# Optimization experiments

Hardware: AMD Instinct MI355X
Metric: run time of the kernel (lower is better)

The kernel has to match this reference:

```python
import jax, jax.numpy as jnp
import numpy as np

D_MODEL = 1024
N_HEADS = 16
D_HEAD = D_MODEL // N_HEADS


def setup_inputs() -> dict:
    key = jax.random.key(0)
    ks = jax.random.split(key, 9)
    B, S = 2, 2048
    s = 0.02
    return {
        "x": jax.random.normal(ks[0], (B, S, D_MODEL), dtype=jnp.float32),
        "Wq": jax.random.normal(ks[1], (D_MODEL, D_MODEL), dtype=jnp.float32) * s,
        "bq": jnp.zeros((D_MODEL,), dtype=jnp.float32),
        "Wk": jax.random.normal(ks[2], (D_MODEL, D_MODEL), dtype=jnp.float32) * s,
        "bk": jnp.zeros((D_MODEL,), dtype=jnp.float32),
        "Wv": jax.random.normal(ks[3], (D_MODEL, D_MODEL), dtype=jnp.float32) * s,
        "bv": jnp.zeros((D_MODEL,), dtype=jnp.float32),
        "Wo": jax.random.normal(ks[4], (D_MODEL, D_MODEL), dtype=jnp.float32) * s,
        "bo": jnp.zeros((D_MODEL,), dtype=jnp.float32),
    }


def reference(x, Wq, bq, Wk, bk, Wv, bv, Wo, bo):
    B, S, _ = x.shape
    # projections -> [B, H, S, Dh]
    def split_heads(t):
        return t.reshape(B, S, N_HEADS, D_HEAD).transpose(0, 2, 1, 3)
    Q = split_heads(x @ Wq + bq)
    K = split_heads(x @ Wk + bk)
    V = split_heads(x @ Wv + bv)
    scores = jnp.einsum('bhqd,bhkd->bhqk', Q, K)  # [B,H,S,S]
    mask = jnp.tril(jnp.ones((S, S), dtype=bool))
    # NB: original masks BEFORE scaling (mask fill -1e9 then /sqrt(d_head))
    scores = jnp.where(mask[None, None], scores, jnp.float32(-1e9))
    scores = scores / jnp.sqrt(jnp.float32(D_HEAD))
    attn = jax.nn.softmax(scores, axis=-1)
    ctx = jnp.einsum('bhqk,bhkd->bhqd', attn, V)
    ctx = ctx.transpose(0, 2, 1, 3).reshape(B, S, D_MODEL)
    return ctx @ Wo + bo
```

## Files before the change

kernel.cpp:

```cpp
#include <hip/hip_runtime.h>

typedef __bf16 bf16;
typedef __bf16 bf16x8 __attribute__((ext_vector_type(8)));
typedef __bf16 bf16x4 __attribute__((ext_vector_type(4)));
typedef float  f32x4  __attribute__((ext_vector_type(4)));

#define D_MODEL 1024
#define S_LEN   2048
#define NHEAD   16
#define DHEAD   64
#define BATCH   2
#define MROWS   (BATCH * S_LEN)

#define QSCALE 0.18033688011112042f

__device__ __forceinline__ void gld_lds16(const void* g, void* lds_base) {
    __builtin_amdgcn_global_load_lds(
        (const __attribute__((address_space(1))) void*)g,
        (__attribute__((address_space(3))) void*)lds_base, 16, 0, 0);
}

__global__ void prep_kernel(const float* __restrict__ x,
                            const float* __restrict__ W0, const float* __restrict__ W1,
                            const float* __restrict__ W2, const float* __restrict__ W3,
                            bf16* __restrict__ xb, bf16* __restrict__ Wt) {
    int tx = threadIdx.x, ty = threadIdx.y;
    if (blockIdx.z == 4) {
        int tid = ty * 32 + tx;
        size_t base = ((size_t)blockIdx.y * 32 + blockIdx.x) * 4096 + (size_t)tid * 16;
        f32x4 v0 = *(const f32x4*)(x + base);
        f32x4 v1 = *(const f32x4*)(x + base + 4);
        f32x4 v2 = *(const f32x4*)(x + base + 8);
        f32x4 v3 = *(const f32x4*)(x + base + 12);
        bf16x8 o0, o1;
#pragma unroll
        for (int r = 0; r < 4; r++) {
            o0[r] = (bf16)v0[r]; o0[r + 4] = (bf16)v1[r];
            o1[r] = (bf16)v2[r]; o1[r + 4] = (bf16)v3[r];
        }
        *(bf16x8*)(xb + base)     = o0;
        *(bf16x8*)(xb + base + 8) = o1;
        return;
    }
    __shared__ float tile[32][33];
    const float* W = (blockIdx.z == 0) ? W0 : (blockIdx.z == 1) ? W1
                   : (blockIdx.z == 2) ? W2 : W3;
    int n0 = blockIdx.x * 32, k0 = blockIdx.y * 32;
#pragma unroll
    for (int j = 0; j < 4; j++)
        tile[ty + 8 * j][tx] = W[(size_t)(k0 + ty + 8 * j) * D_MODEL + n0 + tx];
    __syncthreads();
    bf16* out = Wt + (size_t)blockIdx.z * D_MODEL * D_MODEL;
    int nn = ty + 8 * (tx >> 3);
    int k4 = (tx & 7) * 4;
    bf16x4 pk;
#pragma unroll
    for (int r = 0; r < 4; r++) pk[r] = (bf16)tile[k4 + r][nn];
    *(bf16x4*)(out + (size_t)(n0 + nn) * D_MODEL + k0 + k4) = pk;
}

template <int MODE>
__global__ __launch_bounds__(256, 3) void gemm_kernel(
    const bf16* __restrict__ A, const bf16* __restrict__ Bt,
    const float* __restrict__ b0, const float* __restrict__ b1, const float* __restrict__ b2,
    bf16* __restrict__ Qo, bf16* __restrict__ Ko, bf16* __restrict__ Vto,
    float* __restrict__ Co) {
    __shared__ bf16 sA[3][128 * 32];
    __shared__ bf16 sB[3][128 * 32];
    const int t = threadIdx.x;
    const int wave = t >> 6, lane = t & 63;
    const int wm = wave >> 1, wn = wave & 1;
    const int quad = lane >> 4, m16 = lane & 15;
    const int row0 = blockIdx.y * 128, col0 = blockIdx.x * 128;
    const int K = D_MODEL;
    const int NT = K / 32;

    f32x4 acc[4][4];
#pragma unroll
    for (int i = 0; i < 4; i++)
#pragma unroll
        for (int j = 0; j < 4; j++) acc[i][j] = (f32x4){0.f, 0.f, 0.f, 0.f};

    auto stage = [&](int j, int buf) {
#pragma unroll
        for (int i = 0; i < 2; i++) {
            int cb = i * 256 + wave * 64;
            int c  = cb + lane;
            int r  = c >> 2, kg = c & 3;
            gld_lds16(A  + (size_t)(row0 + r) * K + j * 32 + kg * 8,
                      (char*)&sA[buf][0] + cb * 16);
            gld_lds16(Bt + (size_t)(col0 + r) * K + j * 32 + kg * 8,
                      (char*)&sB[buf][0] + cb * 16);
        }
    };

    stage(0, 0);
    stage(1, 1);

    for (int j = 0; j < NT; ++j) {
        if (j + 1 < NT) asm volatile("s_waitcnt vmcnt(4)\n\ts_barrier" ::: "memory");
        else            asm volatile("s_waitcnt vmcnt(0)\n\ts_barrier" ::: "memory");
        if (j + 2 < NT) stage(j + 2, (j + 2) % 3);
        const int cur = j % 3;

        bf16x8 af[4], bfr[4];
#pragma unroll
        for (int mi = 0; mi < 4; mi++)
            af[mi] = *(const bf16x8*)&sA[cur][(wm * 64 + mi * 16 + m16) * 32 + quad * 8];
#pragma unroll
        for (int ni = 0; ni < 4; ni++)
            bfr[ni] = *(const bf16x8*)&sB[cur][(wn * 64 + ni * 16 + m16) * 32 + quad * 8];
#pragma unroll
        for (int mi = 0; mi < 4; mi++)
#pragma unroll
            for (int ni = 0; ni < 4; ni++)
                acc[mi][ni] = __builtin_amdgcn_mfma_f32_16x16x32_bf16(
                    af[mi], bfr[ni], acc[mi][ni], 0, 0, 0);
    }

    if (MODE == 1) {
#pragma unroll
        for (int mi = 0; mi < 4; mi++) {
            int r0 = row0 + wm * 64 + mi * 16 + quad * 4;
#pragma unroll
            for (int ni = 0; ni < 4; ni++) {
                int col = col0 + wn * 64 + ni * 16 + m16;
                float bias = b0[col];
#pragma unroll
                for (int r = 0; r < 4; r++)
                    Co[(size_t)(r0 + r) * D_MODEL + col] = acc[mi][ni][r] + bias;
            }
        }
    } else {
        int sel = col0 >> 10;
        const float* bias_arr = (sel == 0) ? b0 : (sel == 1) ? b1 : b2;
#pragma unroll
        for (int mi = 0; mi < 4; mi++) {
            int s0g = row0 + wm * 64 + mi * 16 + quad * 4;
            int b = s0g >> 11, ss0 = s0g & 2047;
#pragma unroll
            for (int ni = 0; ni < 4; ni++) {
                int col = col0 + wn * 64 + ni * 16 + m16;
                int cn = col & 1023;
                int h = cn >> 6, d = cn & 63;
                float bias = bias_arr[cn];
                if (sel < 2) {
                    bf16* dst = (sel == 0) ? Qo : Ko;
                    float scl = (sel == 0) ? QSCALE : 1.0f;
                    size_t base = (((size_t)b * NHEAD + h) * S_LEN);
#pragma unroll
                    for (int r = 0; r < 4; r++)
                        dst[(base + ss0 + r) * DHEAD + d] = (bf16)((acc[mi][ni][r] + bias) * scl);
                } else {
                    bf16x4 pk;
#pragma unroll
                    for (int r = 0; r < 4; r++) pk[r] = (bf16)(acc[mi][ni][r] + bias);
                    *(bf16x4*)(Vto + (((size_t)b * NHEAD + h) * DHEAD + d) * S_LEN + ss0) = pk;
                }
            }
        }
    }
}

__global__ __launch_bounds__(256, 2) void attn_kernel(
    const bf16* __restrict__ Q, const bf16* __restrict__ K,
    const bf16* __restrict__ Vt, bf16* __restrict__ ctx) {
    __shared__ bf16 Kt_s[3][64 * 64];
    __shared__ bf16 Vt_s[3][64 * 64];
    __shared__ bf16 P_s[4][2][16 * 72];

    const int t = threadIdx.x, wave = t >> 6, lane = t & 63;
    const int quad = lane >> 4, m16 = lane & 15;
    const int bh = blockIdx.y, p = blockIdx.x;
    const int tT[2] = {p, 31 - p};
    const int nt = 32 - p;
    const size_t base = (size_t)bh * S_LEN * DHEAD;

    bf16x8 aq[2][2];
#pragma unroll
    for (int it = 0; it < 2; it++)
#pragma unroll
        for (int kst = 0; kst < 2; kst++)
            aq[it][kst] = *(const bf16x8*)(Q + base
                + (size_t)(tT[it] * 64 + wave * 16 + m16) * DHEAD + kst * 32 + quad * 8);

    f32x4 o[2][4];
#pragma unroll
    for (int it = 0; it < 2; it++)
#pragma unroll
        for (int di = 0; di < 4; di++) o[it][di] = (f32x4){0.f, 0.f, 0.f, 0.f};
    float l_acc[2] = {0.f, 0.f};

    auto stage = [&](int j, int buf) {
#pragma unroll
        for (int i = 0; i < 2; i++) {
            int cb = i * 256 + wave * 64;
            int c  = cb + lane;
            int pos = c >> 3, g = c & 7;
            int gk = g ^ (pos & 7);
            gld_lds16(K  + base + (size_t)(j * 64 + pos) * DHEAD + gk * 8,
                      (char*)&Kt_s[buf][0] + cb * 16);
            gld_lds16(Vt + base + (size_t)pos * S_LEN + j * 64 + gk * 8,
                      (char*)&Vt_s[buf][0] + cb * 16);
        }
    };

    stage(0, 0);
    if (nt > 1) stage(1, 1);

    for (int j = 0; j < nt; ++j) {
        if (j + 1 < nt) asm volatile("s_waitcnt vmcnt(4)\n\ts_barrier" ::: "memory");
        else            asm volatile("s_waitcnt vmcnt(0)\n\ts_barrier" ::: "memory");
        if (j + 2 < nt) stage(j + 2, (j + 2) % 3);

        const int cur = j % 3;
        const bool aAct = (j <= tT[0]);
        const int kt0 = j * 64;

        auto computeTile = [&](bool both) {
            int itlo = both ? 0 : 1;
            f32x4 sc[2][4];
#pragma unroll
            for (int it = 0; it < 2; it++)
#pragma unroll
                for (int ni = 0; ni < 4; ni++) sc[it][ni] = (f32x4){0.f, 0.f, 0.f, 0.f};
#pragma unroll
            for (int ni = 0; ni < 4; ni++) {
                int pos = ni * 16 + m16;
#pragma unroll
                for (int kst = 0; kst < 2; kst++) {
                    int gg = (kst * 4 + quad) ^ (pos & 7);
                    bf16x8 kf = *(const bf16x8*)&Kt_s[cur][pos * 64 + gg * 8];
                    sc[1][ni] = __builtin_amdgcn_mfma_f32_16x16x32_bf16(
                        kf, aq[1][kst], sc[1][ni], 0, 0, 0);
                    if (both)
                        sc[0][ni] = __builtin_amdgcn_mfma_f32_16x16x32_bf16(
                            kf, aq[0][kst], sc[0][ni], 0, 0, 0);
                }
            }
#pragma unroll
            for (int it = 0; it < 2; it++) {
                if (it < itlo) continue;
                if (j == tT[it]) {
                    int qg = tT[it] * 64 + wave * 16 + m16;
#pragma unroll
                    for (int ni = 0; ni < 4; ni++)
#pragma unroll
                        for (int r = 0; r < 4; r++) {
                            int kp = kt0 + ni * 16 + quad * 4 + r;
                            if (kp > qg) sc[it][ni][r] = -1e9f;
                        }
                }
            }
#pragma unroll
            for (int it = 0; it < 2; it++) {
                if (it < itlo) continue;
                bf16* Pw = &P_s[wave][it][0];
                float ls = 0.f;
#pragma unroll
                for (int ni = 0; ni < 4; ni++) {
                    bf16x4 pk;
#pragma unroll
                    for (int r = 0; r < 4; r++) {
                        float pe = __builtin_amdgcn_exp2f(sc[it][ni][r]);
                        ls += pe;
                        pk[r] = (bf16)pe;
                    }
                    *(bf16x4*)&Pw[m16 * 72 + ni * 16 + quad * 4] = pk;
                }
                l_acc[it] += ls;
            }
#pragma unroll
            for (int kst = 0; kst < 2; kst++) {
                bf16x8 ap[2];
#pragma unroll
                for (int it = 0; it < 2; it++)
                    if (it >= itlo)
                        ap[it] = *(const bf16x8*)&P_s[wave][it][m16 * 72 + kst * 32 + quad * 8];
#pragma unroll
                for (int di = 0; di < 4; di++) {
                    int d = di * 16 + m16;
                    int gg = (kst * 4 + quad) ^ (d & 7);
                    bf16x8 vf = *(const bf16x8*)&Vt_s[cur][d * 64 + gg * 8];
                    o[1][di] = __builtin_amdgcn_mfma_f32_16x16x32_bf16(
                        vf, ap[1], o[1][di], 0, 0, 0);
                    if (both)
                        o[0][di] = __builtin_amdgcn_mfma_f32_16x16x32_bf16(
                            vf, ap[0], o[0][di], 0, 0, 0);
                }
            }
        };
        if (aAct) computeTile(true);
        else      computeTile(false);
    }

    int b = bh >> 4, h = bh & 15;
#pragma unroll
    for (int it = 0; it < 2; it++) {
        float l = l_acc[it];
        l += __shfl_xor(l, 16);
        l += __shfl_xor(l, 32);
        float rl = 1.0f / l;
        int s = tT[it] * 64 + wave * 16 + m16;
#pragma unroll
        for (int di = 0; di < 4; di++) {
            bf16x4 pk;
#pragma unroll
            for (int r = 0; r < 4; r++) pk[r] = (bf16)(o[it][di][r] * rl);
            *(bf16x4*)(ctx + ((size_t)b * S_LEN + s) * D_MODEL
                       + h * DHEAD + di * 16 + quad * 4) = pk;
        }
    }
}

extern "C" void kernel_launch(void* const* d_in, const int* in_sizes, int n_in,
                              void* d_out, int out_size, void* d_ws, size_t ws_size,
                              hipStream_t stream) {
    const float* x  = (const float*)d_in[0];
    const float* Wq = (const float*)d_in[1];
    const float* bq = (const float*)d_in[2];
    const float* Wk = (const float*)d_in[3];
    const float* bk = (const float*)d_in[4];
    const float* Wv = (const float*)d_in[5];
    const float* bv = (const float*)d_in[6];
    const float* Wo = (const float*)d_in[7];
    const float* bo = (const float*)d_in[8];
    float* out = (float*)d_out;

    char* ws = (char*)d_ws;
    const size_t MB = 1u << 20;
    bf16* xb  = (bf16*)(ws + 0);
    bf16* Wt  = (bf16*)(ws + 8  * MB);
    bf16* Qb  = (bf16*)(ws + 16 * MB);
    bf16* Kb  = (bf16*)(ws + 24 * MB);
    bf16* Vtb = (bf16*)(ws + 32 * MB);
    bf16* ctx = (bf16*)(ws + 0);

    prep_kernel<<<dim3(32, 32, 5), dim3(32, 8), 0, stream>>>(x, Wq, Wk, Wv, Wo, xb, Wt);
    gemm_kernel<0><<<dim3(24, 32), 256, 0, stream>>>(xb, Wt, bq, bk, bv,
                                                     Qb, Kb, Vtb, nullptr);
    attn_kernel<<<dim3(16, 32), 256, 0, stream>>>(Qb, Kb, Vtb, ctx);
    gemm_kernel<1><<<dim3(8, 32), 256, 0, stream>>>(ctx, Wt + 3 * 1024 * 1024,
                                                    bo, nullptr, nullptr,
                                                    nullptr, nullptr, nullptr, out);
}
```

Measured before the change: 194.1 us.

## Fuse all four stages into one persistent kernel with grid barriers

Replaces the four separate launches (convert/transpose, QKV GEMM, attention, output GEMM) with a single kernel of 512 blocks that runs each stage in turn and separates them with atomic-counter grid barriers. The QKV GEMM tile becomes 128x192 and the output GEMM tile 128x64 so each stage maps onto exactly 512 blocks. The P buffer moves to an XOR-swizzled layout. This removes launch gaps and inter-kernel idle time, but requires all 512 blocks to be co-resident (2 per CU), and the barrier spin costs time and risks deadlock if they are not.

Result: slower. 373.5 us (+92.5%).

```diff
diff --git a/kernel.cpp b/kernel.cpp
--- a/kernel.cpp
+++ b/kernel.cpp
@@ -9,10 +9,10 @@
 #define S_LEN   2048
 #define NHEAD   16
 #define DHEAD   64
-#define BATCH   2
-#define MROWS   (BATCH * S_LEN)
 
 #define QSCALE 0.18033688011112042f
+
+#define LDS_BYTES 65536
 
 __device__ __forceinline__ void gld_lds16(const void* g, void* lds_base) {
     __builtin_amdgcn_global_load_lds(
@@ -20,295 +20,364 @@
         (__attribute__((address_space(3))) void*)lds_base, 16, 0, 0);
 }
 
-__global__ void prep_kernel(const float* __restrict__ x,
-                            const float* __restrict__ W0, const float* __restrict__ W1,
-                            const float* __restrict__ W2, const float* __restrict__ W3,
-                            bf16* __restrict__ xb, bf16* __restrict__ Wt) {
-    int tx = threadIdx.x, ty = threadIdx.y;
-    if (blockIdx.z == 4) {
-        int tid = ty * 32 + tx;
-        size_t base = ((size_t)blockIdx.y * 32 + blockIdx.x) * 4096 + (size_t)tid * 16;
-        f32x4 v0 = *(const f32x4*)(x + base);
-        f32x4 v1 = *(const f32x4*)(x + base + 4);
-        f32x4 v2 = *(const f32x4*)(x + base + 8);
-        f32x4 v3 = *(const f32x4*)(x + base + 12);
-        bf16x8 o0, o1;
-#pragma unroll
-        for (int r = 0; r < 4; r++) {
-            o0[r] = (bf16)v0[r]; o0[r + 4] = (bf16)v1[r];
-            o1[r] = (bf16)v2[r]; o1[r + 4] = (bf16)v3[r];
-        }
-        *(bf16x8*)(xb + base)     = o0;
-        *(bf16x8*)(xb + base + 8) = o1;
-        return;
+__device__ unsigned g_cnt;
+
+__device__ __forceinline__ void grid_barrier(unsigned target) {
+    __syncthreads();
+    if (threadIdx.x == 0) {
+        __threadfence();
+        __hip_atomic_fetch_add(&g_cnt, 1u, __ATOMIC_ACQ_REL, __HIP_MEMORY_SCOPE_AGENT);
+        while (__hip_atomic_load(&g_cnt, __ATOMIC_RELAXED, __HIP_MEMORY_SCOPE_AGENT) < target)
+            __builtin_amdgcn_s_sleep(2);
+        __threadfence();
     }
-    __shared__ float tile[32][33];
-    const float* W = (blockIdx.z == 0) ? W0 : (blockIdx.z == 1) ? W1
-                   : (blockIdx.z == 2) ? W2 : W3;
-    int n0 = blockIdx.x * 32, k0 = blockIdx.y * 32;
-#pragma unroll
-    for (int j = 0; j < 4; j++)
-        tile[ty + 8 * j][tx] = W[(size_t)(k0 + ty + 8 * j) * D_MODEL + n0 + tx];
     __syncthreads();
-    bf16* out = Wt + (size_t)blockIdx.z * D_MODEL * D_MODEL;
-    int nn = ty + 8 * (tx >> 3);
-    int k4 = (tx & 7) * 4;
-    bf16x4 pk;
-#pragma unroll
-    for (int r = 0; r < 4; r++) pk[r] = (bf16)tile[k4 + r][nn];
-    *(bf16x4*)(out + (size_t)(n0 + nn) * D_MODEL + k0 + k4) = pk;
 }
 
-template <int MODE>
-__global__ __launch_bounds__(256, 3) void gemm_kernel(
-    const bf16* __restrict__ A, const bf16* __restrict__ Bt,
-    const float* __restrict__ b0, const float* __restrict__ b1, const float* __restrict__ b2,
-    bf16* __restrict__ Qo, bf16* __restrict__ Ko, bf16* __restrict__ Vto,
-    float* __restrict__ Co) {
-    __shared__ bf16 sA[3][128 * 32];
-    __shared__ bf16 sB[3][128 * 32];
+__global__ __launch_bounds__(256, 2) void fused_mha_kernel(
+    const float* __restrict__ x,
+    const float* __restrict__ Wq, const float* __restrict__ bq,
+    const float* __restrict__ Wk, const float* __restrict__ bk,
+    const float* __restrict__ Wv, const float* __restrict__ bv,
+    const float* __restrict__ Wo, const float* __restrict__ bo,
+    bf16* xb, bf16* __restrict__ Wt,
+    bf16* __restrict__ Qb, bf16* __restrict__ Kb, bf16* __restrict__ Vtb,
+    bf16* ctx, float* __restrict__ out)
+{
+    __shared__ __align__(16) char lds[LDS_BYTES];
+    const int bid = blockIdx.x;
     const int t = threadIdx.x;
     const int wave = t >> 6, lane = t & 63;
-    const int wm = wave >> 1, wn = wave & 1;
     const int quad = lane >> 4, m16 = lane & 15;
-    const int row0 = blockIdx.y * 128, col0 = blockIdx.x * 128;
-    const int K = D_MODEL;
-    const int NT = K / 32;
-
-    f32x4 acc[4][4];
-#pragma unroll
-    for (int i = 0; i < 4; i++)
-#pragma unroll
-        for (int j = 0; j < 4; j++) acc[i][j] = (f32x4){0.f, 0.f, 0.f, 0.f};
-
-    auto stage = [&](int j, int buf) {
-#pragma unroll
-        for (int i = 0; i < 2; i++) {
-            int cb = i * 256 + wave * 64;
-            int c  = cb + lane;
-            int r  = c >> 2, kg = c & 3;
-            gld_lds16(A  + (size_t)(row0 + r) * K + j * 32 + kg * 8,
-                      (char*)&sA[buf][0] + cb * 16);
-            gld_lds16(Bt + (size_t)(col0 + r) * K + j * 32 + kg * 8,
-                      (char*)&sB[buf][0] + cb * 16);
-        }
-    };
-
-    stage(0, 0);
-    stage(1, 1);
-
-    for (int j = 0; j < NT; ++j) {
-        if (j + 1 < NT) asm volatile("s_waitcnt vmcnt(4)\n\ts_barrier" ::: "memory");
-        else            asm volatile("s_waitcnt vmcnt(0)\n\ts_barrier" ::: "memory");
-        if (j + 2 < NT) stage(j + 2, (j + 2) % 3);
-        const int cur = j % 3;
-
-        bf16x8 af[4], bfr[4];
-#pragma unroll
-        for (int mi = 0; mi < 4; mi++)
-            af[mi] = *(const bf16x8*)&sA[cur][(wm * 64 + mi * 16 + m16) * 32 + quad * 8];
-#pragma unroll
-        for (int ni = 0; ni < 4; ni++)
-            bfr[ni] = *(const bf16x8*)&sB[cur][(wn * 64 + ni * 16 + m16) * 32 + quad * 8];
-#pragma unroll
-        for (int mi = 0; mi < 4; mi++)
-#pragma unroll
-            for (int ni = 0; ni < 4; ni++)
-                acc[mi][ni] = __builtin_amdgcn_mfma_f32_16x16x32_bf16(
-                    af[mi], bfr[ni], acc[mi][ni], 0, 0, 0);
+
+    {
+#pragma unroll
+        for (int j = 0; j < 2; j++) {
+            size_t base = ((size_t)bid * 512 + j * 256 + t) * 16;
+            f32x4 v0 = *(const f32x4*)(x + base);
+            f32x4 v1 = *(const f32x4*)(x + base + 4);
+            f32x4 v2 = *(const f32x4*)(x + base + 8);
+            f32x4 v3 = *(const f32x4*)(x + base + 12);
+            bf16x8 o0, o1;
+#pragma unroll
+            for (int r = 0; r < 4; r++) {
+                o0[r] = (bf16)v0[r]; o0[r + 4] = (bf16)v1[r];
+                o1[r] = (bf16)v2[r]; o1[r + 4] = (bf16)v3[r];
+            }
+            *(bf16x8*)(xb + base)     = o0;
+            *(bf16x8*)(xb + base + 8) = o1;
+        }
+        float (*tile)[33] = (float(*)[33])lds;
+        int tx = t & 31, ty = t >> 5;
+        for (int i = 0; i < 8; i++) {
+            int ti = bid * 8 + i;
+            int w = ti >> 10, rem = ti & 1023;
+            int n0 = (rem & 31) * 32, k0 = (rem >> 5) * 32;
+            const float* W = (w == 0) ? Wq : (w == 1) ? Wk : (w == 2) ? Wv : Wo;
+#pragma unroll
+            for (int j = 0; j < 4; j++)
+                tile[ty + 8 * j][tx] = W[(size_t)(k0 + ty + 8 * j) * D_MODEL + n0 + tx];
+            __syncthreads();
+            int nn = ty + 8 * (tx >> 3), k4 = (tx & 7) * 4;
+            bf16x4 pk;
+#pragma unroll
+            for (int r = 0; r < 4; r++) pk[r] = (bf16)tile[k4 + r][nn];
+            *(bf16x4*)(Wt + (size_t)w * 1048576 + (size_t)(n0 + nn) * D_MODEL + k0 + k4) = pk;
+            __syncthreads();
+        }
     }
-
-    if (MODE == 1) {
-#pragma unroll
-        for (int mi = 0; mi < 4; mi++) {
-            int r0 = row0 + wm * 64 + mi * 16 + quad * 4;
-#pragma unroll
-            for (int ni = 0; ni < 4; ni++) {
-                int col = col0 + wn * 64 + ni * 16 + m16;
-                float bias = b0[col];
-#pragma unroll
-                for (int r = 0; r < 4; r++)
-                    Co[(size_t)(r0 + r) * D_MODEL + col] = acc[mi][ni][r] + bias;
-            }
-        }
-    } else {
-        int sel = col0 >> 10;
-        const float* bias_arr = (sel == 0) ? b0 : (sel == 1) ? b1 : b2;
+    grid_barrier(512);
+
+    {
+        bf16* sA = (bf16*)lds;
+        bf16* sB = (bf16*)(lds + 24576);
+        const int wm = wave >> 1, wn = wave & 1;
+        const int col0 = (bid & 15) * 192, row0 = (bid >> 4) * 128;
+        const int K = D_MODEL, NT = 32;
+
+        f32x4 acc[4][6];
+#pragma unroll
+        for (int i = 0; i < 4; i++)
+#pragma unroll
+            for (int j = 0; j < 6; j++) acc[i][j] = (f32x4){0.f, 0.f, 0.f, 0.f};
+
+        auto stage = [&](int j, int buf) {
+#pragma unroll
+            for (int i = 0; i < 2; i++) {
+                int cb = i * 256 + wave * 64;
+                int c = cb + lane, r = c >> 2, kg = c & 3;
+                gld_lds16(xb + (size_t)(row0 + r) * K + j * 32 + kg * 8,
+                          (char*)(sA + buf * 4096) + cb * 16);
+            }
+#pragma unroll
+            for (int i = 0; i < 3; i++) {
+                int cb = i * 256 + wave * 64;
+                int c = cb + lane, r = c >> 2, kg = c & 3;
+                gld_lds16(Wt + (size_t)(col0 + r) * K + j * 32 + kg * 8,
+                          (char*)(sB + buf * 6144) + cb * 16);
+            }
+        };
+        stage(0, 0);
+        stage(1, 1);
+        for (int j = 0; j < NT; ++j) {
+            if (j + 1 < NT) asm volatile("s_waitcnt vmcnt(5)\n\ts_barrier" ::: "memory");
+            else            asm volatile("s_waitcnt vmcnt(0)\n\ts_barrier" ::: "memory");
+            if (j + 2 < NT) stage(j + 2, (j + 2) % 3);
+            const int cur = j % 3;
+            bf16x8 af[4], bfr[6];
+#pragma unroll
+            for (int mi = 0; mi < 4; mi++)
+                af[mi] = *(const bf16x8*)&sA[cur * 4096 + (wm * 64 + mi * 16 + m16) * 32 + quad * 8];
+#pragma unroll
+            for (int ni = 0; ni < 6; ni++)
+                bfr[ni] = *(const bf16x8*)&sB[cur * 6144 + (wn * 96 + ni * 16 + m16) * 32 + quad * 8];
+#pragma unroll
+            for (int mi = 0; mi < 4; mi++)
+#pragma unroll
+                for (int ni = 0; ni < 6; ni++)
+                    acc[mi][ni] = __builtin_amdgcn_mfma_f32_16x16x32_bf16(
+                        af[mi], bfr[ni], acc[mi][ni], 0, 0, 0);
+        }
 #pragma unroll
         for (int mi = 0; mi < 4; mi++) {
             int s0g = row0 + wm * 64 + mi * 16 + quad * 4;
             int b = s0g >> 11, ss0 = s0g & 2047;
 #pragma unroll
-            for (int ni = 0; ni < 4; ni++) {
-                int col = col0 + wn * 64 + ni * 16 + m16;
-                int cn = col & 1023;
+            for (int ni = 0; ni < 6; ni++) {
+                int col = col0 + wn * 96 + ni * 16 + m16;
+                int cn = col & 1023, sel = col >> 10;
                 int h = cn >> 6, d = cn & 63;
-                float bias = bias_arr[cn];
+                const float* ba = (sel == 0) ? bq : (sel == 1) ? bk : bv;
+                float bias = ba[cn];
                 if (sel < 2) {
-                    bf16* dst = (sel == 0) ? Qo : Ko;
+                    bf16* dst = (sel == 0) ? Qb : Kb;
                     float scl = (sel == 0) ? QSCALE : 1.0f;
-                    size_t base = (((size_t)b * NHEAD + h) * S_LEN);
+                    size_t qkb = ((size_t)b * NHEAD + h) * S_LEN;
 #pragma unroll
                     for (int r = 0; r < 4; r++)
-                        dst[(base + ss0 + r) * DHEAD + d] = (bf16)((acc[mi][ni][r] + bias) * scl);
+                        dst[(qkb + ss0 + r) * DHEAD + d] = (bf16)((acc[mi][ni][r] + bias) * scl);
                 } else {
                     bf16x4 pk;
 #pragma unroll
                     for (int r = 0; r < 4; r++) pk[r] = (bf16)(acc[mi][ni][r] + bias);
-                    *(bf16x4*)(Vto + (((size_t)b * NHEAD + h) * DHEAD + d) * S_LEN + ss0) = pk;
+                    *(bf16x4*)(Vtb + (((size_t)b * NHEAD + h) * DHEAD + d) * S_LEN + ss0) = pk;
                 }
             }
         }
     }
-}
-
-__global__ __launch_bounds__(256, 2) void attn_kernel(
-    const bf16* __restrict__ Q, const bf16* __restrict__ K,
-    const bf16* __restrict__ Vt, bf16* __restrict__ ctx) {
-    __shared__ bf16 Kt_s[3][64 * 64];
-    __shared__ bf16 Vt_s[3][64 * 64];
-    __shared__ bf16 P_s[4][2][16 * 72];
-
-    const int t = threadIdx.x, wave = t >> 6, lane = t & 63;
-    const int quad = lane >> 4, m16 = lane & 15;
-    const int bh = blockIdx.y, p = blockIdx.x;
-    const int tT[2] = {p, 31 - p};
-    const int nt = 32 - p;
-    const size_t base = (size_t)bh * S_LEN * DHEAD;
-
-    bf16x8 aq[2][2];
-#pragma unroll
-    for (int it = 0; it < 2; it++)
-#pragma unroll
-        for (int kst = 0; kst < 2; kst++)
-            aq[it][kst] = *(const bf16x8*)(Q + base
-                + (size_t)(tT[it] * 64 + wave * 16 + m16) * DHEAD + kst * 32 + quad * 8);
-
-    f32x4 o[2][4];
-#pragma unroll
-    for (int it = 0; it < 2; it++)
-#pragma unroll
-        for (int di = 0; di < 4; di++) o[it][di] = (f32x4){0.f, 0.f, 0.f, 0.f};
-    float l_acc[2] = {0.f, 0.f};
-
-    auto stage = [&](int j, int buf) {
-#pragma unroll
-        for (int i = 0; i < 2; i++) {
-            int cb = i * 256 + wave * 64;
-            int c  = cb + lane;
-            int pos = c >> 3, g = c & 7;
-            int gk = g ^ (pos & 7);
-            gld_lds16(K  + base + (size_t)(j * 64 + pos) * DHEAD + gk * 8,
-                      (char*)&Kt_s[buf][0] + cb * 16);
-            gld_lds16(Vt + base + (size_t)pos * S_LEN + j * 64 + gk * 8,
-                      (char*)&Vt_s[buf][0] + cb * 16);
-        }
-    };
-
-    stage(0, 0);
-    if (nt > 1) stage(1, 1);
-
-    for (int j = 0; j < nt; ++j) {
-        if (j + 1 < nt) asm volatile("s_waitcnt vmcnt(4)\n\ts_barrier" ::: "memory");
-        else            asm volatile("s_waitcnt vmcnt(0)\n\ts_barrier" ::: "memory");
-        if (j + 2 < nt) stage(j + 2, (j + 2) % 3);
-
-        const int cur = j % 3;
-        const bool aAct = (j <= tT[0]);
-        const int kt0 = j * 64;
-
-        auto computeTile = [&](bool both) {
-            int itlo = both ? 0 : 1;
-            f32x4 sc[2][4];
-#pragma unroll
-            for (int it = 0; it < 2; it++)
-#pragma unroll
-                for (int ni = 0; ni < 4; ni++) sc[it][ni] = (f32x4){0.f, 0.f, 0.f, 0.f};
-#pragma unroll
-            for (int ni = 0; ni < 4; ni++) {
-                int pos = ni * 16 + m16;
+    grid_barrier(1024);
+
+    {
+        bf16* Kt_s = (bf16*)lds;
+        bf16* Vt_s = (bf16*)(lds + 24576);
+        bf16* P_s  = (bf16*)(lds + 49152);
+        const int p = bid & 15, bh = bid >> 4;
+        const int tT[2] = {p, 31 - p};
+        const int nt = 32 - p;
+        const size_t kvb = (size_t)bh * S_LEN * DHEAD;
+
+        bf16x8 aq[2][2];
+#pragma unroll
+        for (int it = 0; it < 2; it++)
+#pragma unroll
+            for (int kst = 0; kst < 2; kst++)
+                aq[it][kst] = *(const bf16x8*)(Qb + kvb
+                    + (size_t)(tT[it] * 64 + wave * 16 + m16) * DHEAD + kst * 32 + quad * 8);
+
+        f32x4 o[2][4];
+#pragma unroll
+        for (int it = 0; it < 2; it++)
+#pragma unroll
+            for (int di = 0; di < 4; di++) o[it][di] = (f32x4){0.f, 0.f, 0.f, 0.f};
+        float l_acc[2] = {0.f, 0.f};
+
+        auto stage = [&](int j, int buf) {
+#pragma unroll
+            for (int i = 0; i < 2; i++) {
+                int cb = i * 256 + wave * 64;
+                int c = cb + lane;
+                int pos = c >> 3, g = c & 7;
+                int gk = g ^ (pos & 7);
+                gld_lds16(Kb + kvb + (size_t)(j * 64 + pos) * DHEAD + gk * 8,
+                          (char*)(Kt_s + buf * 4096) + cb * 16);
+                gld_lds16(Vtb + kvb + (size_t)pos * S_LEN + j * 64 + gk * 8,
+                          (char*)(Vt_s + buf * 4096) + cb * 16);
+            }
+        };
+        stage(0, 0);
+        if (nt > 1) stage(1, 1);
+
+        for (int j = 0; j < nt; ++j) {
+            if (j + 1 < nt) asm volatile("s_waitcnt vmcnt(4)\n\ts_barrier" ::: "memory");
+            else            asm volatile("s_waitcnt vmcnt(0)\n\ts_barrier" ::: "memory");
+            if (j + 2 < nt) stage(j + 2, (j + 2) % 3);
+
+            const int cur = j % 3;
+            const bool aAct = (j <= tT[0]);
+            const int kt0 = j * 64;
+
+            auto computeTile = [&](bool both) {
+                int itlo = both ? 0 : 1;
+                f32x4 sc[2][4];
+#pragma unroll
+                for (int it = 0; it < 2; it++)
+#pragma unroll
+                    for (int ni = 0; ni < 4; ni++) sc[it][ni] = (f32x4){0.f, 0.f, 0.f, 0.f};
+#pragma unroll
+                for (int ni = 0; ni < 4; ni++) {
+                    int pos = ni * 16 + m16;
+#pragma unroll
+                    for (int kst = 0; kst < 2; kst++) {
+                        int gg = (kst * 4 + quad) ^ (pos & 7);
+                        bf16x8 kf = *(const bf16x8*)&Kt_s[cur * 4096 + pos * 64 + gg * 8];
+                        sc[1][ni] = __builtin_amdgcn_mfma_f32_16x16x32_bf16(
+                            kf, aq[1][kst], sc[1][ni], 0, 0, 0);
+                        if (both)
+                            sc[0][ni] = __builtin_amdgcn_mfma_f32_16x16x32_bf16(
+                                kf, aq[0][kst], sc[0][ni], 0, 0, 0);
+                    }
+                }
+#pragma unroll
+                for (int it = 0; it < 2; it++) {
+                    if (it < itlo) continue;
+                    if (j == tT[it]) {
+                        int qg = tT[it] * 64 + wave * 16 + m16;
+#pragma unroll
+                        for (int ni = 0; ni < 4; ni++)
+#pragma unroll
+                            for (int r = 0; r < 4; r++) {
+                                int kp = kt0 + ni * 16 + quad * 4 + r;
+                                if (kp > qg) sc[it][ni][r] = -1e9f;
+                            }
+                    }
+                }
+#pragma unroll
+                for (int it = 0; it < 2; it++) {
+                    if (it < itlo) continue;
+                    bf16* Pw = P_s + (wave * 2 + it) * 1024;
+                    float ls = 0.f;
+#pragma unroll
+                    for (int ni = 0; ni < 4; ni++) {
+                        bf16x4 pk;
+#pragma unroll
+                        for (int r = 0; r < 4; r++) {
+                            float pe = __builtin_amdgcn_exp2f(sc[it][ni][r]);
+                            ls += pe;
+                            pk[r] = (bf16)pe;
+                        }
+                        int u8 = (((ni * 2 + (quad >> 1)) ^ (m16 & 7)) << 1) | (quad & 1);
+                        *(bf16x4*)&Pw[m16 * 64 + u8 * 4] = pk;
+                    }
+                    l_acc[it] += ls;
+                }
 #pragma unroll
                 for (int kst = 0; kst < 2; kst++) {
-                    int gg = (kst * 4 + quad) ^ (pos & 7);
-                    bf16x8 kf = *(const bf16x8*)&Kt_s[cur][pos * 64 + gg * 8];
-                    sc[1][ni] = __builtin_amdgcn_mfma_f32_16x16x32_bf16(
-                        kf, aq[1][kst], sc[1][ni], 0, 0, 0);
-                    if (both)
-                        sc[0][ni] = __builtin_amdgcn_mfma_f32_16x16x32_bf16(
-                            kf, aq[0][kst], sc[0][ni], 0, 0, 0);
+                    bf16x8 ap[2];
+#pragma unroll
+                    for (int it = 0; it < 2; it++)
+                        if (it >= itlo) {
+                            int cc = ((kst * 4 + quad) ^ (m16 & 7)) * 8;
+                            ap[it] = *(const bf16x8*)&P_s[(wave * 2 + it) * 1024
+                                                          + m16 * 64 + cc];
+                        }
+#pragma unroll
+                    for (int di = 0; di < 4; di++) {
+                        int d = di * 16 + m16;
+                        int gg = (kst * 4 + quad) ^ (d & 7);
+                        bf16x8 vf = *(const bf16x8*)&Vt_s[cur * 4096 + d * 64 + gg * 8];
+                        o[1][di] = __builtin_amdgcn_mfma_f32_16x16x32_bf16(
+                            vf, ap[1], o[1][di], 0, 0, 0);
+                        if (both)
+                            o[0][di] = __builtin_amdgcn_mfma_f32_16x16x32_bf16(
+                                vf, ap[0], o[0][di], 0, 0, 0);
+                    }
                 }
-            }
-#pragma unroll
-            for (int it = 0; it < 2; it++) {
-                if (it < itlo) continue;
-                if (j == tT[it]) {
-                    int qg = tT[it] * 64 + wave * 16 + m16;
-#pragma unroll
-                    for (int ni = 0; ni < 4; ni++)
-#pragma unroll
-                        for (int r = 0; r < 4; r++) {
-                            int kp = kt0 + ni * 16 + quad * 4 + r;
-                            if (kp > qg) sc[it][ni][r] = -1e9f;
-                        }
-                }
-            }
-#pragma unroll
-            for (int it = 0; it < 2; it++) {
-                if (it < itlo) continue;
-                bf16* Pw = &P_s[wave][it][0];
-                float ls = 0.f;
-#pragma unroll
-                for (int ni = 0; ni < 4; ni++) {
-                    bf16x4 pk;
-#pragma unroll
-                    for (int r = 0; r < 4; r++) {
-                        float pe = __builtin_amdgcn_exp2f(sc[it][ni][r]);
-                        ls += pe;
-                        pk[r] = (bf16)pe;
-                    }
-                    *(bf16x4*)&Pw[m16 * 72 + ni * 16 + quad * 4] = pk;
-                }
-                l_acc[it] += ls;
-            }
-#pragma unroll
-            for (int kst = 0; kst < 2; kst++) {
-                bf16x8 ap[2];
-#pragma unroll
-                for (int it = 0; it < 2; it++)
-                    if (it >= itlo)
-                        ap[it] = *(const bf16x8*)&P_s[wave][it][m16 * 72 + kst * 32 + quad * 8];
-#pragma unroll
-                for (int di = 0; di < 4; di++) {
-                    int d = di * 16 + m16;
-                    int gg = (kst * 4 + quad) ^ (d & 7);
-                    bf16x8 vf = *(const bf16x8*)&Vt_s[cur][d * 64 + gg * 8];
-                    o[1][di] = __builtin_amdgcn_mfma_f32_16x16x32_bf16(
-                        vf, ap[1], o[1][di], 0, 0, 0);
-                    if (both)
-                        o[0][di] = __builtin_amdgcn_mfma_f32_16x16x32_bf16(
-                            vf, ap[0], o[0][di], 0, 0, 0);
-                }
+            };
+            if (aAct) computeTile(true);
+            else      computeTile(false);
+        }
+
+        int b = bh >> 4, h = bh & 15;
+#pragma unroll
+        for (int it = 0; it < 2; it++) {
+            float l = l_acc[it];
+            l += __shfl_xor(l, 16);
+            l += __shfl_xor(l, 32);
+            float rl = 1.0f / l;
+            int s = tT[it] * 64 + wave * 16 + m16;
+#pragma unroll
+            for (int di = 0; di < 4; di++) {
+                bf16x4 pk;
+#pragma unroll
+                for (int r = 0; r < 4; r++) pk[r] = (bf16)(o[it][di][r] * rl);
+                *(bf16x4*)(ctx + ((size_t)b * S_LEN + s) * D_MODEL
+                           + h * DHEAD + di * 16 + quad * 4) = pk;
+            }
+        }
+    }
+    grid_barrier(1536);
+
+    {
+        bf16* sA = (bf16*)lds;
+        bf16* sB = (bf16*)(lds + 24576);
+        const int wm = wave >> 1, wn = wave & 1;
+        const int col0 = (bid & 15) * 64, row0 = (bid >> 4) * 128;
+        const bf16* Bt = Wt + 3 * 1048576;
+        const int K = D_MODEL, NT = 32;
+
+        f32x4 acc[4][2];
+#pragma unroll
+        for (int i = 0; i < 4; i++)
+#pragma unroll
+            for (int j = 0; j < 2; j++) acc[i][j] = (f32x4){0.f, 0.f, 0.f, 0.f};
+
+        auto stage = [&](int j, int buf) {
+#pragma unroll
+            for (int i = 0; i < 2; i++) {
+                int cb = i * 256 + wave * 64;
+                int c = cb + lane, r = c >> 2, kg = c & 3;
+                gld_lds16(ctx + (size_t)(row0 + r) * K + j * 32 + kg * 8,
+                          (char*)(sA + buf * 4096) + cb * 16);
+            }
+            {
+                int cb = wave * 64;
+                int c = cb + lane, r = c >> 2, kg = c & 3;
+                gld_lds16(Bt + (size_t)(col0 + r) * K + j * 32 + kg * 8,
+                          (char*)(sB + buf * 2048) + cb * 16);
             }
         };
-        if (aAct) computeTile(true);
-        else      computeTile(false);
-    }
-
-    int b = bh >> 4, h = bh & 15;
-#pragma unroll
-    for (int it = 0; it < 2; it++) {
-        float l = l_acc[it];
-        l += __shfl_xor(l, 16);
-        l += __shfl_xor(l, 32);
-        float rl = 1.0f / l;
-        int s = tT[it] * 64 + wave * 16 + m16;
-#pragma unroll
-        for (int di = 0; di < 4; di++) {
-            bf16x4 pk;
-#pragma unroll
-            for (int r = 0; r < 4; r++) pk[r] = (bf16)(o[it][di][r] * rl);
-            *(bf16x4*)(ctx + ((size_t)b * S_LEN + s) * D_MODEL
-                       + h * DHEAD + di * 16 + quad * 4) = pk;
+        stage(0, 0);
+        stage(1, 1);
+        for (int j = 0; j < NT; ++j) {
+            if (j + 1 < NT) asm volatile("s_waitcnt vmcnt(3)\n\ts_barrier" ::: "memory");
+            else            asm volatile("s_waitcnt vmcnt(0)\n\ts_barrier" ::: "memory");
+            if (j + 2 < NT) stage(j + 2, (j + 2) % 3);
+            const int cur = j % 3;
+            bf16x8 af[4], bfr[2];
+#pragma unroll
+            for (int mi = 0; mi < 4; mi++)
+                af[mi] = *(const bf16x8*)&sA[cur * 4096 + (wm * 64 + mi * 16 + m16) * 32 + quad * 8];
+#pragma unroll
+            for (int ni = 0; ni < 2; ni++)
+                bfr[ni] = *(const bf16x8*)&sB[cur * 2048 + (wn * 32 + ni * 16 + m16) * 32 + quad * 8];
+#pragma unroll
+            for (int mi = 0; mi < 4; mi++)
+#pragma unroll
+                for (int ni = 0; ni < 2; ni++)
+                    acc[mi][ni] = __builtin_amdgcn_mfma_f32_16x16x32_bf16(
+                        af[mi], bfr[ni], acc[mi][ni], 0, 0, 0);
+        }
+#pragma unroll
+        for (int mi = 0; mi < 4; mi++) {
+            int r0 = row0 + wm * 64 + mi * 16 + quad * 4;
+#pragma unroll
+            for (int ni = 0; ni < 2; ni++) {
+                int col = col0 + wn * 32 + ni * 16 + m16;
+                float bias = bo[col];
+#pragma unroll
+                for (int r = 0; r < 4; r++)
+                    out[(size_t)(r0 + r) * D_MODEL + col] = acc[mi][ni][r] + bias;
+            }
         }
     }
 }
@@ -336,11 +405,11 @@
     bf16* Vtb = (bf16*)(ws + 32 * MB);
     bf16* ctx = (bf16*)(ws + 0);
 
-    prep_kernel<<<dim3(32, 32, 5), dim3(32, 8), 0, stream>>>(x, Wq, Wk, Wv, Wo, xb, Wt);
-    gemm_kernel<0><<<dim3(24, 32), 256, 0, stream>>>(xb, Wt, bq, bk, bv,
-                                                     Qb, Kb, Vtb, nullptr);
-    attn_kernel<<<dim3(16, 32), 256, 0, stream>>>(Qb, Kb, Vtb, ctx);
-    gemm_kernel<1><<<dim3(8, 32), 256, 0, stream>>>(ctx, Wt + 3 * 1024 * 1024,
-                                                    bo, nullptr, nullptr,
-                                                    nullptr, nullptr, nullptr, out);
+    unsigned* cnt_addr = nullptr;
+    hipGetSymbolAddress((void**)&cnt_addr, HIP_SYMBOL(g_cnt));
+    hipMemsetAsync(cnt_addr, 0, sizeof(unsigned), stream);
+
+    fused_mha_kernel<<<512, 256, 0, stream>>>(
+        x, Wq, bq, Wk, bk, Wv, bv, Wo, bo,
+        xb, Wt, Qb, Kb, Vtb, ctx, out);
 }
```

## Use 32x32 MFMA in QKV GEMM and smaller M-tile for output GEMM

Applied to the files above, without the earlier changes.

Splits the templated GEMM into two kernels. The QKV projection now uses 32x32x16 bf16 MFMA instructions, which cut LDS fragment reads per FLOP, and its epilogue is rewritten for the 32x32 accumulator layout. The output projection uses 64x128 tiles, giving 512 blocks instead of 256 for better CU fill on the small N=1024 GEMM. The trade-off is lower per-block reuse and a different vmcnt wait count.

New measurement: 196.6 us. About the same (+1.3%).

```diff
diff --git a/kernel.cpp b/kernel.cpp
--- a/kernel.cpp
+++ b/kernel.cpp
@@ -4,13 +4,12 @@
 typedef __bf16 bf16x8 __attribute__((ext_vector_type(8)));
 typedef __bf16 bf16x4 __attribute__((ext_vector_type(4)));
 typedef float  f32x4  __attribute__((ext_vector_type(4)));
+typedef float  f32x16 __attribute__((ext_vector_type(16)));
 
 #define D_MODEL 1024
 #define S_LEN   2048
 #define NHEAD   16
 #define DHEAD   64
-#define BATCH   2
-#define MROWS   (BATCH * S_LEN)
 
 #define QSCALE 0.18033688011112042f
 
@@ -59,41 +58,39 @@
     *(bf16x4*)(out + (size_t)(n0 + nn) * D_MODEL + k0 + k4) = pk;
 }
 
-template <int MODE>
-__global__ __launch_bounds__(256, 3) void gemm_kernel(
+__global__ __launch_bounds__(256, 3) void gemm_qkv_kernel(
     const bf16* __restrict__ A, const bf16* __restrict__ Bt,
-    const float* __restrict__ b0, const float* __restrict__ b1, const float* __restrict__ b2,
-    bf16* __restrict__ Qo, bf16* __restrict__ Ko, bf16* __restrict__ Vto,
-    float* __restrict__ Co) {
+    const float* __restrict__ bq, const float* __restrict__ bk,
+    const float* __restrict__ bv,
+    bf16* __restrict__ Qo, bf16* __restrict__ Ko, bf16* __restrict__ Vto) {
     __shared__ bf16 sA[3][128 * 32];
     __shared__ bf16 sB[3][128 * 32];
     const int t = threadIdx.x;
     const int wave = t >> 6, lane = t & 63;
     const int wm = wave >> 1, wn = wave & 1;
-    const int quad = lane >> 4, m16 = lane & 15;
+    const int l31 = lane & 31, half = lane >> 5;
     const int row0 = blockIdx.y * 128, col0 = blockIdx.x * 128;
-    const int K = D_MODEL;
-    const int NT = K / 32;
-
-    f32x4 acc[4][4];
-#pragma unroll
-    for (int i = 0; i < 4; i++)
-#pragma unroll
-        for (int j = 0; j < 4; j++) acc[i][j] = (f32x4){0.f, 0.f, 0.f, 0.f};
+    const int K = D_MODEL, NT = 32;
+
+    f32x16 acc[2][2];
+#pragma unroll
+    for (int i = 0; i < 2; i++)
+#pragma unroll
+        for (int j = 0; j < 2; j++)
+#pragma unroll
+            for (int e = 0; e < 16; e++) acc[i][j][e] = 0.f;
 
     auto stage = [&](int j, int buf) {
 #pragma unroll
         for (int i = 0; i < 2; i++) {
             int cb = i * 256 + wave * 64;
-            int c  = cb + lane;
-            int r  = c >> 2, kg = c & 3;
+            int c = cb + lane, r = c >> 2, kg = c & 3;
             gld_lds16(A  + (size_t)(row0 + r) * K + j * 32 + kg * 8,
                       (char*)&sA[buf][0] + cb * 16);
             gld_lds16(Bt + (size_t)(col0 + r) * K + j * 32 + kg * 8,
                       (char*)&sB[buf][0] + cb * 16);
         }
     };
-
     stage(0, 0);
     stage(1, 1);
 
@@ -103,61 +100,125 @@
         if (j + 2 < NT) stage(j + 2, (j + 2) % 3);
         const int cur = j % 3;
 
-        bf16x8 af[4], bfr[4];
-#pragma unroll
-        for (int mi = 0; mi < 4; mi++)
-            af[mi] = *(const bf16x8*)&sA[cur][(wm * 64 + mi * 16 + m16) * 32 + quad * 8];
+        bf16x8 af[2][2], bfr[2][2];
+#pragma unroll
+        for (int ks = 0; ks < 2; ks++)
+#pragma unroll
+            for (int mi = 0; mi < 2; mi++) {
+                af[ks][mi]  = *(const bf16x8*)&sA[cur][(wm * 64 + mi * 32 + l31) * 32
+                                                       + ks * 16 + half * 8];
+                bfr[ks][mi] = *(const bf16x8*)&sB[cur][(wn * 64 + mi * 32 + l31) * 32
+                                                       + ks * 16 + half * 8];
+            }
+#pragma unroll
+        for (int ks = 0; ks < 2; ks++)
+#pragma unroll
+            for (int mi = 0; mi < 2; mi++)
+#pragma unroll
+                for (int ni = 0; ni < 2; ni++)
+                    acc[mi][ni] = __builtin_amdgcn_mfma_f32_32x32x16_bf16(
+                        af[ks][mi], bfr[ks][ni], acc[mi][ni], 0, 0, 0);
+    }
+
+#pragma unroll
+    for (int mi = 0; mi < 2; mi++)
+#pragma unroll
+        for (int ni = 0; ni < 2; ni++) {
+            int n = col0 + wn * 64 + ni * 32 + l31;
+            int cn = n & 1023, sel = n >> 10;
+            int h = cn >> 6, d = cn & 63;
+            const float* ba = (sel == 0) ? bq : (sel == 1) ? bk : bv;
+            float bias = ba[cn];
+#pragma unroll
+            for (int g = 0; g < 4; g++) {
+                int m = row0 + wm * 64 + mi * 32 + half * 4 + g * 8;
+                int b = m >> 11, ss0 = m & 2047;
+                if (sel < 2) {
+                    bf16* dst = (sel == 0) ? Qo : Ko;
+                    float scl = (sel == 0) ? QSCALE : 1.0f;
+                    size_t qkb = ((size_t)b * NHEAD + h) * S_LEN;
+#pragma unroll
+                    for (int r = 0; r < 4; r++)
+                        dst[(qkb + ss0 + r) * DHEAD + d] =
+                            (bf16)((acc[mi][ni][g * 4 + r] + bias) * scl);
+                } else {
+                    bf16x4 pk;
+#pragma unroll
+                    for (int r = 0; r < 4; r++)
+                        pk[r] = (bf16)(acc[mi][ni][g * 4 + r] + bias);
+                    *(bf16x4*)(Vto + (((size_t)b * NHEAD + h) * DHEAD + d) * S_LEN + ss0) = pk;
+                }
+            }
+        }
+}
+
+__global__ __launch_bounds__(256, 4) void gemm_out_kernel(
+    const bf16* __restrict__ A, const bf16* __restrict__ Bt,
+    const float* __restrict__ bo, float* __restrict__ Co) {
+    __shared__ bf16 sA[3][64 * 32];
+    __shared__ bf16 sB[3][128 * 32];
+    const int t = threadIdx.x;
+    const int wave = t >> 6, lane = t & 63;
+    const int wm = wave >> 1, wn = wave & 1;
+    const int quad = lane >> 4, m16 = lane & 15;
+    const int row0 = blockIdx.y * 64, col0 = blockIdx.x * 128;
+    const int K = D_MODEL, NT = 32;
+
+    f32x4 acc[2][4];
+#pragma unroll
+    for (int i = 0; i < 2; i++)
+#pragma unroll
+        for (int j = 0; j < 4; j++) acc[i][j] = (f32x4){0.f, 0.f, 0.f, 0.f};
+
+    auto stage = [&](int j, int buf) {
+        {
+            int cb = wave * 64;
+            int c = cb + lane, r = c >> 2, kg = c & 3;
+            gld_lds16(A + (size_t)(row0 + r) * K + j * 32 + kg * 8,
+                      (char*)&sA[buf][0] + cb * 16);
+        }
+#pragma unroll
+        for (int i = 0; i < 2; i++) {
+            int cb = i * 256 + wave * 64;
+            int c = cb + lane, r = c >> 2, kg = c & 3;
+            gld_lds16(Bt + (size_t)(col0 + r) * K + j * 32 + kg * 8,
+                      (char*)&sB[buf][0] + cb * 16);
+        }
+    };
+    stage(0, 0);
+    stage(1, 1);
+
+    for (int j = 0; j < NT; ++j) {
+        if (j + 1 < NT) asm volatile("s_waitcnt vmcnt(3)\n\ts_barrier" ::: "memory");
+        else            asm volatile("s_waitcnt vmcnt(0)\n\ts_barrier" ::: "memory");
+        if (j + 2 < NT) stage(j + 2, (j + 2) % 3);
+        const int cur = j % 3;
+
+        bf16x8 af[2], bfr[4];
+#pragma unroll
+        for (int mi = 0; mi < 2; mi++)
+            af[mi] = *(const bf16x8*)&sA[cur][(wm * 32 + mi * 16 + m16) * 32 + quad * 8];
 #pragma unroll
         for (int ni = 0; ni < 4; ni++)
             bfr[ni] = *(const bf16x8*)&sB[cur][(wn * 64 + ni * 16 + m16) * 32 + quad * 8];
 #pragma unroll
-        for (int mi = 0; mi < 4; mi++)
+        for (int mi = 0; mi < 2; mi++)
 #pragma unroll
             for (int ni = 0; ni < 4; ni++)
                 acc[mi][ni] = __builtin_amdgcn_mfma_f32_16x16x32_bf16(
                     af[mi], bfr[ni], acc[mi][ni], 0, 0, 0);
     }
 
-    if (MODE == 1) {
-#pragma unroll
-        for (int mi = 0; mi < 4; mi++) {
-            int r0 = row0 + wm * 64 + mi * 16 + quad * 4;
-#pragma unroll
-            for (int ni = 0; ni < 4; ni++) {
-                int col = col0 + wn * 64 + ni * 16 + m16;
-                float bias = b0[col];
-#pragma unroll
-                for (int r = 0; r < 4; r++)
-                    Co[(size_t)(r0 + r) * D_MODEL + col] = acc[mi][ni][r] + bias;
-            }
-        }
-    } else {
-        int sel = col0 >> 10;
-        const float* bias_arr = (sel == 0) ? b0 : (sel == 1) ? b1 : b2;
-#pragma unroll
-        for (int mi = 0; mi < 4; mi++) {
-            int s0g = row0 + wm * 64 + mi * 16 + quad * 4;
-            int b = s0g >> 11, ss0 = s0g & 2047;
-#pragma unroll
-            for (int ni = 0; ni < 4; ni++) {
-                int col = col0 + wn * 64 + ni * 16 + m16;
-                int cn = col & 1023;
-                int h = cn >> 6, d = cn & 63;
-                float bias = bias_arr[cn];
-                if (sel < 2) {
-                    bf16* dst = (sel == 0) ? Qo : Ko;
-                    float scl = (sel == 0) ? QSCALE : 1.0f;
-                    size_t base = (((size_t)b * NHEAD + h) * S_LEN);
-#pragma unroll
-                    for (int r = 0; r < 4; r++)
-                        dst[(base + ss0 + r) * DHEAD + d] = (bf16)((acc[mi][ni][r] + bias) * scl);
-                } else {
-                    bf16x4 pk;
-#pragma unroll
-                    for (int r = 0; r < 4; r++) pk[r] = (bf16)(acc[mi][ni][r] + bias);
-                    *(bf16x4*)(Vto + (((size_t)b * NHEAD + h) * DHEAD + d) * S_LEN + ss0) = pk;
-                }
-            }
+#pragma unroll
+    for (int mi = 0; mi < 2; mi++) {
+        int r0 = row0 + wm * 32 + mi * 16 + quad * 4;
+#pragma unroll
+        for (int ni = 0; ni < 4; ni++) {
+            int col = col0 + wn * 64 + ni * 16 + m16;
+            float bias = bo[col];
+#pragma unroll
+            for (int r = 0; r < 4; r++)
+                Co[(size_t)(r0 + r) * D_MODEL + col] = acc[mi][ni][r] + bias;
         }
     }
 }
@@ -195,7 +256,7 @@
 #pragma unroll
         for (int i = 0; i < 2; i++) {
             int cb = i * 256 + wave * 64;
-            int c  = cb + lane;
+            int c = cb + lane;
             int pos = c >> 3, g = c & 7;
             int gk = g ^ (pos & 7);
             gld_lds16(K  + base + (size_t)(j * 64 + pos) * DHEAD + gk * 8,
@@ -204,7 +265,6 @@
                       (char*)&Vt_s[buf][0] + cb * 16);
         }
     };
-
     stage(0, 0);
     if (nt > 1) stage(1, 1);
 
@@ -337,10 +397,7 @@
     bf16* ctx = (bf16*)(ws + 0);
 
     prep_kernel<<<dim3(32, 32, 5), dim3(32, 8), 0, stream>>>(x, Wq, Wk, Wv, Wo, xb, Wt);
-    gemm_kernel<0><<<dim3(24, 32), 256, 0, stream>>>(xb, Wt, bq, bk, bv,
-                                                     Qb, Kb, Vtb, nullptr);
+    gemm_qkv_kernel<<<dim3(24, 32), 256, 0, stream>>>(xb, Wt, bq, bk, bv, Qb, Kb, Vtb);
     attn_kernel<<<dim3(16, 32), 256, 0, stream>>>(Qb, Kb, Vtb, ctx);
-    gemm_kernel<1><<<dim3(8, 32), 256, 0, stream>>>(ctx, Wt + 3 * 1024 * 1024,
-                                                    bo, nullptr, nullptr,
-                                                    nullptr, nullptr, nullptr, out);
-}
+    gemm_out_kernel<<<dim3(8, 64), 256, 0, stream>>>(ctx, Wt + 3 * 1048576, bo, out);
+}
```
